# Kernel tuning notes

Hardware: AMD Instinct MI355X
Metric: run time of the kernel (lower is better)

The kernel has to match this reference:

```python
import jax, jax.numpy as jnp
import numpy as np

EPS = 1e-4          # eps in build_deterministic_repr
TEMPERING = 0.1     # self.tempering
GUMBEL_TEMP = 0.1   # temperature in sample_gumbel_softmax
GUMBEL_EPS = 1e-8


def _conv1d(x, w, b, stride=2):
    # x: (N, Cin, L), w: (Cout, Cin, K)  -> valid conv, stride 2 (matches nn.Conv1d)
    y = jax.lax.conv_general_dilated(x, w, window_strides=(stride,), padding='VALID',
                                     dimension_numbers=('NCH', 'OIH', 'NCH'))
    return y + b[None, :, None]


def setup_inputs() -> dict:
    key = jax.random.key(0)
    ks = jax.random.split(key, 12)
    nb, G, C, ch, nmix, hdim, ns = 8, 2048, 512, 8, 4, 10, 10
    xc = jax.random.uniform(ks[0], (nb, C, 1, ch), minval=-2.0, maxval=2.0)
    yc = jax.random.normal(ks[1], (nb, C, ch))
    # xgrid is a linspace over the data range (build_xgrid), broadcast to all dims/channels
    xgrid = jnp.broadcast_to(jnp.linspace(-3.0, 3.0, G)[None, :, None, None],
                             (nb, G, 1, ch)).astype(jnp.float32)
    log_ls = 0.1 * jax.random.normal(ks[2], (ch,))
    w1 = 0.1 * jax.random.normal(ks[3], (hdim, ch, 5));  b1 = jnp.zeros((hdim,))
    w2 = 0.1 * jax.random.normal(ks[4], (hdim, hdim, 5)); b2 = jnp.zeros((hdim,))
    w3 = 0.1 * jax.random.normal(ks[5], (hdim, hdim, 5)); b3 = jnp.zeros((hdim,))
    w4 = 0.1 * jax.random.normal(ks[6], (hdim, hdim, 5)); b4 = jnp.zeros((hdim,))
    wl = 0.1 * jax.random.normal(ks[7], (nmix * ch, hdim)); bl = jnp.zeros((nmix * ch,))
    unif = jax.random.uniform(ks[8], (nb, ns, ch, nmix), minval=1e-6, maxval=1.0)
    return dict(xc=xc, yc=yc, xgrid=xgrid, log_ls=log_ls,
                w1=w1, b1=b1, w2=w2, b2=b2, w3=w3, b3=b3, w4=w4, b4=b4,
                wl=wl, bl=bl, unif=unif)


def reference(xc, yc, xgrid, log_ls, w1, b1, w2, b2, w3, b3, w4, b4, wl, bl, unif):
    nb, G, _, ch = xgrid.shape
    ls = jnp.exp(log_ls)                                    # per-channel RBF lengthscale
    # ---- build_deterministic_repr: RBF Kxt + density / weighted datarepr ----
    # d2[b,g,c,H] = sum_dim (xgrid - xc)^2
    d2 = ((xgrid[:, :, None, :, :] - xc[:, None, :, :, :]) ** 2).sum(axis=3)  # (nb,G,C,ch)
    K = jnp.exp(-0.5 * d2 / (ls ** 2))                      # (nb,G,C,ch)
    density = K.sum(axis=2)                                 # (nb,G,ch)
    datarepr = jnp.einsum('bgcH,bcH->bgH', K, yc) / (density + EPS)  # (nb,G,ch)
    # ---- build_mixweight: weight net on detached datarepr ----
    x = jnp.transpose(jax.lax.stop_gradient(datarepr), (0, 2, 1))   # (nb,ch,G)
    h = jax.nn.relu(_conv1d(x, w1, b1))
    h = jax.nn.relu(_conv1d(h, w2, b2))
    h = jax.nn.relu(_conv1d(h, w3, b3))
    h = _conv1d(h, w4, b4)
    h = h.mean(axis=-1)                                     # AdaptiveAvgPool1d(1)
    logit = h @ wl.T + bl                                   # (nb, nmix*ch)
    logit = logit.reshape(nb, ch, -1)                       # (nb,ch,nmix)
    logit = (logit - logit.max(axis=-1, keepdims=True)) / TEMPERING
    mixweight = jax.nn.softmax(logit, axis=-1)
    # ---- sample_gumbel_softmax on the tempered logits ----
    g = -jnp.log(-jnp.log(unif + GUMBEL_EPS))               # (nb,ns,ch,nmix)
    hh = (g + logit[:, None, :, :]) / GUMBEL_TEMP
    y = jax.nn.softmax(hh - hh.max(axis=-1, keepdims=True), axis=-1)
    mixweight_sample = jnp.clip(y, GUMBEL_EPS, 1.0 - GUMBEL_EPS)
    return density, datarepr, mixweight, mixweight_sample
```

## Files before the change

### kernel.cpp

```cpp
#include <hip/hip_runtime.h>
#include <hip/hip_bf16.h>

#define NB 8
#define G  2048
#define C  512
#define CH 8
#define NM 4
#define HD 10
#define NS 10
#define L1 1022
#define L2 509
#define L3 253
#define L4 125

__global__ __launch_bounds__(256) void k_density(
    const float* __restrict__ xc, const float* __restrict__ yc,
    const float* __restrict__ xg, const float* __restrict__ logls,
    float* __restrict__ out_den,
    float* __restrict__ out_rep)
{
    __shared__ float sden[4][64];
    __shared__ float snum[4][64];
    const int tid  = threadIdx.x;
    const int wave = tid >> 6;
    const int lane = tid & 63;
    const int id = blockIdx.x;
    const int gt = id & 31;
    const int H  = (id >> 5) & 7;
    const int b  = id >> 8;

    const int g = gt * 64 + lane;
    const float x = xg[(b * G + g) * CH + H];
    const float coef = -0.72134752044448170f * __expf(-2.0f * logls[H]);

    const float* xcb = xc + (b * C + wave * 128) * CH + H;
    const float* ycb = yc + (b * C + wave * 128) * CH + H;

    float den = 0.0f, num = 0.0f;
    #pragma unroll 8
    for (int c = 0; c < 128; ++c) {
        const float xx = xcb[c * CH];
        const float yy = ycb[c * CH];
        const float d = x - xx;
        const float w = __builtin_amdgcn_exp2f((d * coef) * d);
        den += w;
        num = fmaf(w, yy, num);
    }

    sden[wave][lane] = den;
    snum[wave][lane] = num;
    __syncthreads();

    if (tid < 64) {
        const float dtot = sden[0][tid] + sden[1][tid] + sden[2][tid] + sden[3][tid];
        const float ntot = snum[0][tid] + snum[1][tid] + snum[2][tid] + snum[3][tid];
        const int o = (b * G + gt * 64 + tid) * CH + H;
        out_den[o] = dtot;
        out_rep[o] = ntot / (dtot + 1e-4f);
    }
}

__global__ __launch_bounds__(256) void k_convnet(
    const float* __restrict__ rep,
    const float* __restrict__ w1, const float* __restrict__ b1,
    const float* __restrict__ w2, const float* __restrict__ b2,
    const float* __restrict__ w3, const float* __restrict__ b3,
    const float* __restrict__ w4, const float* __restrict__ b4,
    float* __restrict__ h4out)
{
    const int b   = blockIdx.x / 25;
    const int t   = blockIdx.x % 25;
    const int tid = threadIdx.x;

    __shared__ float sxt[CH * 125];
    __shared__ float sw1[5 * CH * HD];
    __shared__ float sw2[5 * HD * HD];
    __shared__ float sw3[5 * HD * HD];
    __shared__ float sw4[5 * HD * HD];
    __shared__ float s1[HD * 61];
    __shared__ float s2[HD * 29];
    __shared__ float s3[HD * 13];

    {
        const float* src = rep + (b * G + 80 * t) * CH;
        for (int i = tid; i < 125 * CH; i += 256) {
            const int gl = i >> 3, ci = i & 7;
            sxt[ci * 125 + gl] = src[i];
        }
    }
    for (int i = tid; i < HD * CH * 5; i += 256) {
        const int o = i / 40, ci = (i / 5) % 8, k = i % 5;
        sw1[(k * CH + ci) * HD + o] = w1[i];
    }
    for (int i = tid; i < HD * HD * 5; i += 256) {
        const int o = i / 50, ci = (i / 5) % 10, k = i % 5;
        sw2[(k * HD + ci) * HD + o] = w2[i];
        sw3[(k * HD + ci) * HD + o] = w3[i];
        sw4[(k * HD + ci) * HD + o] = w4[i];
    }
    __syncthreads();

    for (int i = tid; i < 61 * HD; i += 256) {
        const int o = i % HD, ll = i / HD;
        float acc = b1[o];
        #pragma unroll
        for (int k = 0; k < 5; ++k)
            #pragma unroll
            for (int ci = 0; ci < CH; ++ci)
                acc = fmaf(sxt[ci * 125 + 2 * ll + k], sw1[(k * CH + ci) * HD + o], acc);
        s1[o * 61 + ll] = fmaxf(acc, 0.0f);
    }
    __syncthreads();

    for (int i = tid; i < 29 * HD; i += 256) {
        const int o = i % HD, ll = i / HD;
        float acc = b2[o];
        #pragma unroll
        for (int k = 0; k < 5; ++k)
            #pragma unroll
            for (int ci = 0; ci < HD; ++ci)
                acc = fmaf(s1[ci * 61 + 2 * ll + k], sw2[(k * HD + ci) * HD + o], acc);
        s2[o * 29 + ll] = fmaxf(acc, 0.0f);
    }
    __syncthreads();

    for (int i = tid; i < 13 * HD; i += 256) {
        const int o = i % HD, ll = i / HD;
        float acc = b3[o];
        #pragma unroll
        for (int k = 0; k < 5; ++k)
            #pragma unroll
            for (int ci = 0; ci < HD; ++ci)
                acc = fmaf(s2[ci * 29 + 2 * ll + k], sw3[(k * HD + ci) * HD + o], acc);
        s3[o * 13 + ll] = fmaxf(acc, 0.0f);
    }
    __syncthreads();

    for (int i = tid; i < 5 * HD; i += 256) {
        const int o = i % HD, ll = i / HD;
        float acc = b4[o];
        #pragma unroll
        for (int k = 0; k < 5; ++k)
            #pragma unroll
            for (int ci = 0; ci < HD; ++ci)
                acc = fmaf(s3[ci * 13 + 2 * ll + k], sw4[(k * HD + ci) * HD + o], acc);
        h4out[(b * HD + o) * L4 + 5 * t + ll] = acc;
    }
}

__global__ __launch_bounds__(256) void k_tail(
    const float* __restrict__ h4,
    const float* __restrict__ wl, const float* __restrict__ bl,
    const float* __restrict__ unif,
    float* __restrict__ out_mw,
    float* __restrict__ out_ms)
{
    const int b   = blockIdx.x;
    const int tid = threadIdx.x;
    __shared__ float red[HD * 25];
    __shared__ float hm[HD];
    __shared__ float lg[CH * NM];
    __shared__ float ltt[CH * NM];

    if (tid < HD * 25) {
        const int o = tid / 25, j = tid % 25;
        const float* p = h4 + (b * HD + o) * L4 + j * 5;
        red[tid] = p[0] + p[1] + p[2] + p[3] + p[4];
    }
    __syncthreads();
    if (tid < HD) {
        float s = 0.0f;
        #pragma unroll
        for (int j = 0; j < 25; ++j) s += red[tid * 25 + j];
        hm[tid] = s * (1.0f / (float)L4);
    }
    __syncthreads();
    if (tid < CH * NM) {
        float acc = bl[tid];
        #pragma unroll
        for (int k = 0; k < HD; ++k) acc = fmaf(wl[tid * HD + k], hm[k], acc);
        lg[tid] = acc;
    }
    __syncthreads();
    if (tid < CH) {
        float lv[NM];
        #pragma unroll
        for (int m = 0; m < NM; ++m) lv[m] = lg[tid * NM + m];
        const float m0 = fmaxf(fmaxf(lv[0], lv[1]), fmaxf(lv[2], lv[3]));
        float e[NM], s = 0.0f;
        #pragma unroll
        for (int m = 0; m < NM; ++m) {
            const float v = (lv[m] - m0) / 0.1f;
            ltt[tid * NM + m] = v;
            e[m] = __expf(v);
            s += e[m];
        }
        #pragma unroll
        for (int m = 0; m < NM; ++m)
            out_mw[(b * CH + tid) * NM + m] = e[m] / s;
    }
    __syncthreads();
    if (tid < NS * CH) {
        const int c = tid % CH, sI = tid / CH;
        const float* up = unif + ((b * NS + sI) * CH + c) * NM;
        float hh[NM], mx = -1e30f;
        #pragma unroll
        for (int m = 0; m < NM; ++m) {
            const float gu = -__logf(-__logf(up[m] + 1e-8f));
            hh[m] = (gu + ltt[c * NM + m]) / 0.1f;
            mx = fmaxf(mx, hh[m]);
        }
        float e2[NM], ss = 0.0f;
        #pragma unroll
        for (int m = 0; m < NM; ++m) { e2[m] = __expf(hh[m] - mx); ss += e2[m]; }
        #pragma unroll
        for (int m = 0; m < NM; ++m) {
            float y = e2[m] / ss;
            y = fminf(fmaxf(y, 1e-8f), 1.0f - 1e-8f);
            out_ms[((b * NS + sI) * CH + c) * NM + m] = y;
        }
    }
}

extern "C" void kernel_launch(void* const* d_in, const int* in_sizes, int n_in,
                              void* d_out, int out_size, void* d_ws, size_t ws_size,
                              hipStream_t stream) {
    const float* xc    = (const float*)d_in[0];
    const float* yc    = (const float*)d_in[1];
    const float* xg    = (const float*)d_in[2];
    const float* logls = (const float*)d_in[3];
    const float* w1    = (const float*)d_in[4];
    const float* b1    = (const float*)d_in[5];
    const float* w2    = (const float*)d_in[6];
    const float* b2    = (const float*)d_in[7];
    const float* w3    = (const float*)d_in[8];
    const float* b3    = (const float*)d_in[9];
    const float* w4    = (const float*)d_in[10];
    const float* b4    = (const float*)d_in[11];
    const float* wl    = (const float*)d_in[12];
    const float* bl    = (const float*)d_in[13];
    const float* unif  = (const float*)d_in[14];

    float* out = (float*)d_out;
    float* out_den = out;
    float* out_rep = out + NB * G * CH;
    float* out_mw  = out + 2 * NB * G * CH;
    float* out_ms  = out_mw + NB * CH * NM;
    (void)out_size; (void)in_sizes; (void)n_in; (void)ws_size;

    float* ws_h4 = (float*)d_ws;

    k_density<<<2048, 256, 0, stream>>>(xc, yc, xg, logls, out_den, out_rep);

    k_convnet<<<NB * 25, 256, 0, stream>>>(out_rep, w1, b1, w2, b2, w3, b3, w4, b4,
                                           ws_h4);

    k_tail<<<NB, 256, 0, stream>>>(ws_h4, wl, bl, unif, out_mw, out_ms);
}
```

Before: 31.51 us.

## Pack context points into per-channel float4 with precomputed quadratic term

Adds a pre-pass kernel that rearranges xc/yc into contiguous per-(batch,channel) float4 records holding x, y and coef*x^2. The density kernel then reads these records through a wave-uniform (readfirstlane) pointer, so the loads can become scalar/broadcast loads instead of strided per-lane gathers. It also expands the squared distance into A + B*x + coef*x^2, which removes a subtract and a multiply per pair. The cost is one extra kernel launch, more workspace, and slightly different floating-point rounding from the expanded form, which can lose precision through cancellation.

```diff
diff --git a/kernel.cpp b/kernel.cpp
--- a/kernel.cpp
+++ b/kernel.cpp
@@ -13,8 +13,24 @@
 #define L3 253
 #define L4 125
 
+__global__ __launch_bounds__(256) void k_pack(
+    const float* __restrict__ xc, const float* __restrict__ yc,
+    const float* __restrict__ logls,
+    float4* __restrict__ pk)
+{
+    const int idx = blockIdx.x * 256 + threadIdx.x;
+    const int c  = idx & (C - 1);
+    const int bH = idx >> 9;
+    const int H  = bH & 7;
+    const int b  = bH >> 3;
+    const float coef = -0.72134752044448170f * __expf(-2.0f * logls[H]);
+    const float xx = xc[(b * C + c) * CH + H];
+    const float yy = yc[(b * C + c) * CH + H];
+    pk[idx] = make_float4(xx, yy, coef * xx * xx, 0.0f);
+}
+
 __global__ __launch_bounds__(256) void k_density(
-    const float* __restrict__ xc, const float* __restrict__ yc,
+    const float4* __restrict__ pk,
     const float* __restrict__ xg, const float* __restrict__ logls,
     float* __restrict__ out_den,
     float* __restrict__ out_rep)
@@ -22,8 +38,8 @@
     __shared__ float sden[4][64];
     __shared__ float snum[4][64];
     const int tid  = threadIdx.x;
-    const int wave = tid >> 6;
     const int lane = tid & 63;
+    const int wv   = __builtin_amdgcn_readfirstlane(tid >> 6);
     const int id = blockIdx.x;
     const int gt = id & 31;
     const int H  = (id >> 5) & 7;
@@ -32,23 +48,24 @@
     const int g = gt * 64 + lane;
     const float x = xg[(b * G + g) * CH + H];
     const float coef = -0.72134752044448170f * __expf(-2.0f * logls[H]);
-
-    const float* xcb = xc + (b * C + wave * 128) * CH + H;
-    const float* ycb = yc + (b * C + wave * 128) * CH + H;
+    const float A = coef * x * x;
+    const float B = -2.0f * coef * x;
+
+    const int pkoff = __builtin_amdgcn_readfirstlane((b * CH + H) * C + wv * 128);
+    const float4* pkw = pk + pkoff;
 
     float den = 0.0f, num = 0.0f;
     #pragma unroll 8
     for (int c = 0; c < 128; ++c) {
-        const float xx = xcb[c * CH];
-        const float yy = ycb[c * CH];
-        const float d = x - xx;
-        const float w = __builtin_amdgcn_exp2f((d * coef) * d);
+        const float4 v = pkw[c];
+        const float arg = fmaf(v.x, B, A) + v.z;
+        const float w = __builtin_amdgcn_exp2f(arg);
         den += w;
-        num = fmaf(w, yy, num);
-    }
-
-    sden[wave][lane] = den;
-    snum[wave][lane] = num;
+        num = fmaf(w, v.y, num);
+    }
+
+    sden[wv][lane] = den;
+    snum[wv][lane] = num;
     __syncthreads();
 
     if (tid < 64) {
@@ -248,9 +265,12 @@
     float* out_ms  = out_mw + NB * CH * NM;
     (void)out_size; (void)in_sizes; (void)n_in; (void)ws_size;
 
-    float* ws_h4 = (float*)d_ws;
-
-    k_density<<<2048, 256, 0, stream>>>(xc, yc, xg, logls, out_den, out_rep);
+    float4* pk   = (float4*)d_ws;
+    float*  ws_h4 = (float*)d_ws + 4 * 32768;
+
+    k_pack<<<128, 256, 0, stream>>>(xc, yc, logls, pk);
+
+    k_density<<<2048, 256, 0, stream>>>(pk, xg, logls, out_den, out_rep);
 
     k_convnet<<<NB * 25, 256, 0, stream>>>(out_rep, w1, b1, w2, b2, w3, b3, w4, b4,
                                            ws_h4);
```

Measured after the change: 33.72 us. 7.0% more time.
